# Kernel optimization log

Hardware: AMD Instinct MI355X
Metric: run time of the kernel (lower is better)

The kernel has to match this reference:

```python
import jax, jax.numpy as jnp
import numpy as np

MARGIN = 1.0
MAX_TRIALS = 50


def setup_inputs() -> dict:
    key = jax.random.key(0)
    k1, k2 = jax.random.split(key)
    B = 1048576
    scores = jax.random.normal(k1, (B,), dtype=jnp.float32)
    labels = jax.random.randint(k2, (B,), 0, 2, dtype=jnp.int64)
    return {"scores": scores, "labels": labels}


def reference(scores, labels):
    # Vectorized WARP: the sequential rejection-sampling loop draws i.i.d.
    # uniform negatives until a margin violation; equivalently we pre-draw
    # max_trials negatives per example and take the first violating one.
    B = scores.shape[0]
    lab = labels.astype(jnp.int32)
    num_pos = jnp.sum(lab == 1)
    num_neg = jnp.sum(lab == 0)

    # stable argsort puts label-0 (negative) positions first
    order = jnp.argsort(lab)

    key = jax.random.key(42)
    u = jax.random.uniform(key, (B, MAX_TRIALS), dtype=jnp.float32)
    # uniform index into the negative pool (num_neg is traced -> use floor(u*n))
    idx = jnp.minimum((u * num_neg.astype(jnp.float32)).astype(jnp.int32),
                      jnp.maximum(num_neg - 1, 0))
    neg_idx = order[idx]                       # (B, T) positions of sampled negatives
    neg_samples = scores[neg_idx]              # (B, T)

    violates = neg_samples + MARGIN > scores[:, None]   # (B, T)
    any_viol = jnp.any(violates, axis=1)
    trials = jnp.argmax(violates, axis=1)      # number of failed trials before hit
    neg_at = jnp.take_along_axis(neg_samples, trials[:, None], axis=1)[:, 0]

    # rank_est = max(1, max_trials // (trials + 1)); weight = H(rank_est)
    rank_est = jnp.maximum(1, MAX_TRIALS // (trials + 1))
    harmonics = jnp.cumsum(1.0 / jnp.arange(1, MAX_TRIALS + 1, dtype=scores.dtype))
    weight = harmonics[rank_est - 1]

    per = weight * jnp.maximum(MARGIN - (scores - neg_at), 0.0)
    per = jnp.where((lab == 1) & any_viol, per, 0.0)
    total = jnp.sum(per)

    valid = (num_pos > 0) & (num_neg > 0)
    return jnp.where(valid, total / jnp.maximum(num_pos, 1).astype(scores.dtype), 0.0)
```

## Files before the change

kernel.cpp:

```cpp
#include <hip/hip_runtime.h>
#include <stdint.h>

#define MAX_TRIALS 50
#define MARGIN 1.0f

#define SBLOCK 256
#define SEG 1024
#define MBLOCK 1024
#define MME 2
#define MCHUNK (MBLOCK * MME)

#define FLAG_AGG 1ULL
#define FLAG_INC 2ULL

__device__ __forceinline__ uint32_t rotl32(uint32_t x, uint32_t d) {
  return (x << d) | (x >> (32u - d));
}

__device__ __forceinline__ uint32_t threefry_0_42(uint32_t x0, uint32_t x1, int which) {
  const uint32_t k0 = 0u, k1 = 42u;
  const uint32_t k2 = k0 ^ k1 ^ 0x1BD11BDAu;
  const uint32_t ks[3] = {k0, k1, k2};
  const uint32_t rotA[4] = {13u, 15u, 26u, 6u};
  const uint32_t rotB[4] = {17u, 29u, 16u, 24u};
  x0 += ks[0];
  x1 += ks[1];
#pragma unroll
  for (int r = 0; r < 5; ++r) {
#pragma unroll
    for (int j = 0; j < 4; ++j) {
      uint32_t rot = (r & 1) ? rotB[j] : rotA[j];
      x0 += x1;
      x1 = rotl32(x1, rot);
      x1 ^= x0;
    }
    x0 += ks[(r + 1) % 3];
    x1 += ks[(r + 2) % 3] + (uint32_t)(r + 1);
  }
  return which ? x1 : x0;
}

__device__ __forceinline__ float sample_u(uint32_t j, uint32_t half) {
  uint32_t x0, x1;
  int which;
  if (j < half) { x0 = j; x1 = j + half; which = 0; }
  else          { x0 = j - half; x1 = j; which = 1; }
  uint32_t bits = threefry_0_42(x0, x1, which);
  return __uint_as_float((bits >> 9) | 0x3f800000u) - 1.0f;
}

__global__ void __launch_bounds__(SBLOCK) scan_scatter_kernel(
    const float* __restrict__ scores, const int* __restrict__ labels,
    unsigned long long* __restrict__ desc, int* __restrict__ counters,
    float* __restrict__ negScores, float* __restrict__ out, int B, int nseg) {
  __shared__ int s_scan[SBLOCK];
  __shared__ int s_base;
  const int t = threadIdx.x;
  const int seg = blockIdx.x;

  if (seg == 0 && t == 0) out[0] = 0.0f;

  int e0 = seg * SEG + 4 * t;
  int lab[4] = {1, 1, 1, 1};
  float sc[4] = {0.f, 0.f, 0.f, 0.f};
  if (e0 + 3 < B) {
    int4 L = *reinterpret_cast<const int4*>(labels + e0);
    float4 S = *reinterpret_cast<const float4*>(scores + e0);
    lab[0] = L.x; lab[1] = L.y; lab[2] = L.z; lab[3] = L.w;
    sc[0] = S.x; sc[1] = S.y; sc[2] = S.z; sc[3] = S.w;
  } else {
    for (int k = 0; k < 4; ++k) {
      int e = e0 + k;
      if (e < B) { lab[k] = labels[e]; sc[k] = scores[e]; }
    }
  }
  int c = (lab[0] == 0) + (lab[1] == 0) + (lab[2] == 0) + (lab[3] == 0);
  s_scan[t] = c;
  __syncthreads();
  for (int d = 1; d < SBLOCK; d <<= 1) {
    int v = (t >= d) ? s_scan[t - d] : 0;
    __syncthreads();
    s_scan[t] += v;
    __syncthreads();
  }
  const int cnt = s_scan[SBLOCK - 1];

  if (seg == 0) {
    if (t == 0) {
      atomicExch(&desc[0], (FLAG_INC << 32) | (unsigned)cnt);
      s_base = 0;
      if (nseg == 1) counters[0] = cnt;
    }
  } else {
    if (t == 0) atomicExch(&desc[seg], (FLAG_AGG << 32) | (unsigned)cnt);
    if (t < 64) {
      int running = 0;
      int w = 0;
      bool done = false;
      while (!done) {
        int idx = seg - 1 - w * 64 - t;
        unsigned flag;
        int val;
        do {
          if (idx >= 0) {
            unsigned long long v = atomicAdd(&desc[idx], 0ULL);
            flag = (unsigned)(v >> 32);
            val = (int)(unsigned)v;
          } else {
            flag = (unsigned)FLAG_INC;
            val = 0;
          }
        } while (!__all(flag == 1u || flag == 2u));
        unsigned long long incmask = __ballot(flag == 2u);
        int contrib;
        if (incmask) {
          int l = __ffsll(incmask) - 1;
          contrib = (t <= l) ? val : 0;
          done = true;
        } else {
          contrib = val;
          ++w;
        }
#pragma unroll
        for (int off = 32; off > 0; off >>= 1) contrib += __shfl_down(contrib, off, 64);
        if (t == 0) running += contrib;
      }
      if (t == 0) {
        atomicExch(&desc[seg], (FLAG_INC << 32) | (unsigned)(running + cnt));
        s_base = running;
        if (seg == nseg - 1) counters[0] = running + cnt;
      }
    }
  }
  __syncthreads();
  const int base = s_base;

  int pos = base + s_scan[t] - c;
  for (int k = 0; k < 4; ++k)
    if (lab[k] == 0) negScores[pos++] = sc[k];
}

__global__ void __launch_bounds__(MBLOCK, 8) warp_main(
    const float* __restrict__ scores, const int* __restrict__ labels,
    const float* __restrict__ negScores, const int* __restrict__ counters,
    float* __restrict__ out, int B) {
  __shared__ float H[MAX_TRIALS + 1];
  __shared__ int s_qe[MCHUNK];
  __shared__ float s_qs[MCHUNK];
  __shared__ int s_qn;
  __shared__ float s_bsum[MBLOCK / 64];

  const int tid = threadIdx.x;
  const int lane = tid & 63;
  const int wave = tid >> 6;

  if (tid == 0) {
    float a = 0.0f;
    for (int k = 1; k <= MAX_TRIALS; ++k) { a += 1.0f / (float)k; H[k] = a; }
    s_qn = 0;
  }
  __syncthreads();

  const int num_neg = counters[0];
  if (num_neg == 0) return;

  const float fneg = (float)num_neg;
  const uint32_t half = (uint32_t)(((unsigned long long)B * MAX_TRIALS) >> 1);

  float acc = 0.0f;
  int my_e[MME];
  float my_s[MME];
  int nsurv = 0;

  int e0 = blockIdx.x * MCHUNK + 2 * tid;
  int lab[2] = {1, 1};
  float sc[2] = {0.f, 0.f};
  if (e0 + 1 < B) {
    int2 L = *reinterpret_cast<const int2*>(labels + e0);
    float2 S = *reinterpret_cast<const float2*>(scores + e0);
    lab[0] = L.x; lab[1] = L.y;
    sc[0] = S.x; sc[1] = S.y;
  } else {
    for (int k = 0; k < 2; ++k) {
      int e = e0 + k;
      if (e < B) { lab[k] = labels[e]; sc[k] = scores[e]; }
    }
  }
  float n0[2], n1[2];
#pragma unroll
  for (int k = 0; k < 2; ++k) {
    if (lab[k] == 1) {
      uint32_t jb = (uint32_t)(e0 + k) * (uint32_t)MAX_TRIALS;
      float u0 = sample_u(jb, half);
      float u1 = sample_u(jb + 1u, half);
      int i0 = (int)(u0 * fneg);
      int i1 = (int)(u1 * fneg);
      if (i0 > num_neg - 1) i0 = num_neg - 1;
      if (i1 > num_neg - 1) i1 = num_neg - 1;
      n0[k] = negScores[i0];
      n1[k] = negScores[i1];
    }
  }
#pragma unroll
  for (int k = 0; k < 2; ++k) {
    if (lab[k] == 1) {
      float s = sc[k];
      if (n0[k] + MARGIN > s) {
        float h = MARGIN - (s - n0[k]);
        if (h < 0.0f) h = 0.0f;
        acc += H[50] * h;
      } else if (n1[k] + MARGIN > s) {
        float h = MARGIN - (s - n1[k]);
        if (h < 0.0f) h = 0.0f;
        acc += H[25] * h;
      } else {
        my_e[nsurv] = e0 + k;
        my_s[nsurv] = s;
        ++nsurv;
      }
    }
  }

  int qp = 0;
  if (nsurv) qp = atomicAdd(&s_qn, nsurv);
  for (int i = 0; i < nsurv; ++i) {
    s_qe[qp + i] = my_e[i];
    s_qs[qp + i] = my_s[i];
  }
  __syncthreads();

  const int qn = s_qn;
  for (int q = wave; q < qn; q += MBLOCK / 64) {
    float sq = s_qs[q];
    int eq = s_qe[q];
    int t = 2 + lane;
    bool viol = false;
    float neg = 0.0f;
    if (t < MAX_TRIALS) {
      float u = sample_u((uint32_t)eq * (uint32_t)MAX_TRIALS + (uint32_t)t, half);
      int idx = (int)(u * fneg);
      if (idx > num_neg - 1) idx = num_neg - 1;
      neg = negScores[idx];
      viol = (neg + MARGIN > sq);
    }
    unsigned long long vm = __ballot(viol);
    if (vm) {
      int f = __ffsll(vm) - 1;
      if (lane == f) {
        int trials = 2 + f;
        int rank = MAX_TRIALS / (trials + 1);
        if (rank < 1) rank = 1;
        float h = MARGIN - (sq - neg);
        if (h < 0.0f) h = 0.0f;
        acc += H[rank] * h;
      }
    }
  }

  float v = acc;
#pragma unroll
  for (int off = 32; off > 0; off >>= 1) v += __shfl_down(v, off, 64);
  if (lane == 0) s_bsum[wave] = v;
  __syncthreads();
  if (tid == 0) {
    int np = B - num_neg;
    if (np > 0) {
      float bs = 0.0f;
      for (int i = 0; i < MBLOCK / 64; ++i) bs += s_bsum[i];
      atomicAdd(out, bs * (1.0f / (float)np));
    }
  }
}

extern "C" void kernel_launch(void* const* d_in, const int* in_sizes, int n_in,
                              void* d_out, int out_size, void* d_ws, size_t ws_size,
                              hipStream_t stream) {
  const float* scores = (const float*)d_in[0];
  const int* labels = (const int*)d_in[1];
  int B = in_sizes[0];
  int nseg = (B + SEG - 1) / SEG;
  int nb2 = (B + MCHUNK - 1) / MCHUNK;

  char* ws = (char*)d_ws;
  int* counters = (int*)ws;
  unsigned long long* desc = (unsigned long long*)(ws + 64);
  float* negScores = (float*)(ws + 64 + 8 * 1024);

  scan_scatter_kernel<<<nseg, SBLOCK, 0, stream>>>(scores, labels, desc, counters,
                                                   negScores, (float*)d_out, B, nseg);
  warp_main<<<nb2, MBLOCK, 0, stream>>>(scores, labels, negScores, counters,
                                        (float*)d_out, B);
}
```

Before: 89.53 us.

## Compact positive examples during scan and spread them evenly across main-kernel blocks

After: 94.09 us. 5.1% more time.

```diff
diff --git a/kernel.cpp b/kernel.cpp
--- a/kernel.cpp
+++ b/kernel.cpp
@@ -52,7 +52,8 @@
 __global__ void __launch_bounds__(SBLOCK) scan_scatter_kernel(
     const float* __restrict__ scores, const int* __restrict__ labels,
     unsigned long long* __restrict__ desc, int* __restrict__ counters,
-    float* __restrict__ negScores, float* __restrict__ out, int B, int nseg) {
+    float* __restrict__ negScores, int* __restrict__ posE,
+    float* __restrict__ posS, float* __restrict__ out, int B, int nseg) {
   __shared__ int s_scan[SBLOCK];
   __shared__ int s_base;
   const int t = threadIdx.x;
@@ -135,13 +136,24 @@
   __syncthreads();
   const int base = s_base;
 
-  int pos = base + s_scan[t] - c;
-  for (int k = 0; k < 4; ++k)
-    if (lab[k] == 0) negScores[pos++] = sc[k];
+  int negRank = base + s_scan[t] - c;
+  for (int k = 0; k < 4; ++k) {
+    int e = e0 + k;
+    if (e < B) {
+      if (lab[k] == 0) {
+        negScores[negRank] = sc[k];
+        ++negRank;
+      } else {
+        int pi = e - negRank;
+        posE[pi] = e;
+        posS[pi] = sc[k];
+      }
+    }
+  }
 }
 
 __global__ void __launch_bounds__(MBLOCK, 8) warp_main(
-    const float* __restrict__ scores, const int* __restrict__ labels,
+    const int* __restrict__ posE, const float* __restrict__ posS,
     const float* __restrict__ negScores, const int* __restrict__ counters,
     float* __restrict__ out, int B) {
   __shared__ float H[MAX_TRIALS + 1];
@@ -163,48 +175,57 @@
 
   const int num_neg = counters[0];
   if (num_neg == 0) return;
+  const int np = B - num_neg;
+  if (np <= 0) return;
 
   const float fneg = (float)num_neg;
   const uint32_t half = (uint32_t)(((unsigned long long)B * MAX_TRIALS) >> 1);
+
+  const int nb = (int)gridDim.x;
+  int chunk = (((np + nb - 1) / nb) + 1) & ~1;
+  const int p0 = blockIdx.x * chunk;
+  const int p1 = min(p0 + chunk, np);
 
   float acc = 0.0f;
   int my_e[MME];
   float my_s[MME];
   int nsurv = 0;
 
-  int e0 = blockIdx.x * MCHUNK + 2 * tid;
-  int lab[2] = {1, 1};
-  float sc[2] = {0.f, 0.f};
-  if (e0 + 1 < B) {
-    int2 L = *reinterpret_cast<const int2*>(labels + e0);
-    float2 S = *reinterpret_cast<const float2*>(scores + e0);
-    lab[0] = L.x; lab[1] = L.y;
-    sc[0] = S.x; sc[1] = S.y;
+  const int i0 = p0 + 2 * tid;
+  int pe[2];
+  float ps[2];
+  bool val[2] = {false, false};
+  if (i0 + 1 < p1) {
+    int2 E = *reinterpret_cast<const int2*>(posE + i0);
+    float2 S = *reinterpret_cast<const float2*>(posS + i0);
+    pe[0] = E.x; pe[1] = E.y;
+    ps[0] = S.x; ps[1] = S.y;
+    val[0] = val[1] = true;
   } else {
     for (int k = 0; k < 2; ++k) {
-      int e = e0 + k;
-      if (e < B) { lab[k] = labels[e]; sc[k] = scores[e]; }
-    }
-  }
+      if (i0 + k < p1) { pe[k] = posE[i0 + k]; ps[k] = posS[i0 + k]; val[k] = true; }
+    }
+  }
+
   float n0[2], n1[2];
 #pragma unroll
   for (int k = 0; k < 2; ++k) {
-    if (lab[k] == 1) {
-      uint32_t jb = (uint32_t)(e0 + k) * (uint32_t)MAX_TRIALS;
+    if (val[k]) {
+      uint32_t jb = (uint32_t)pe[k] * (uint32_t)MAX_TRIALS;
       float u0 = sample_u(jb, half);
       float u1 = sample_u(jb + 1u, half);
-      int i0 = (int)(u0 * fneg);
-      int i1 = (int)(u1 * fneg);
-      if (i0 > num_neg - 1) i0 = num_neg - 1;
-      if (i1 > num_neg - 1) i1 = num_neg - 1;
-      n0[k] = negScores[i0];
-      n1[k] = negScores[i1];
+      int g0 = (int)(u0 * fneg);
+      int g1 = (int)(u1 * fneg);
+      if (g0 > num_neg - 1) g0 = num_neg - 1;
+      if (g1 > num_neg - 1) g1 = num_neg - 1;
+      n0[k] = negScores[g0];
+      n1[k] = negScores[g1];
     }
   }
 #pragma unroll
   for (int k = 0; k < 2; ++k) {
-    if (lab[k] == 1) {
-      float s = sc[k];
+    if (val[k]) {
+      float s = ps[k];
       if (n0[k] + MARGIN > s) {
         float h = MARGIN - (s - n0[k]);
         if (h < 0.0f) h = 0.0f;
@@ -214,7 +235,7 @@
         if (h < 0.0f) h = 0.0f;
         acc += H[25] * h;
       } else {
-        my_e[nsurv] = e0 + k;
+        my_e[nsurv] = pe[k];
         my_s[nsurv] = s;
         ++nsurv;
       }
@@ -263,12 +284,9 @@
   if (lane == 0) s_bsum[wave] = v;
   __syncthreads();
   if (tid == 0) {
-    int np = B - num_neg;
-    if (np > 0) {
-      float bs = 0.0f;
-      for (int i = 0; i < MBLOCK / 64; ++i) bs += s_bsum[i];
-      atomicAdd(out, bs * (1.0f / (float)np));
-    }
+    float bs = 0.0f;
+    for (int i = 0; i < MBLOCK / 64; ++i) bs += s_bsum[i];
+    atomicAdd(out, bs * (1.0f / (float)np));
   }
 }
 
@@ -284,10 +302,14 @@
   char* ws = (char*)d_ws;
   int* counters = (int*)ws;
   unsigned long long* desc = (unsigned long long*)(ws + 64);
-  float* negScores = (float*)(ws + 64 + 8 * 1024);
+  char* p = ws + 64 + 8192;
+  int* posE = (int*)p;
+  float* posS = (float*)(p + (size_t)B * 4);
+  float* negScores = (float*)(p + (size_t)B * 8);
 
   scan_scatter_kernel<<<nseg, SBLOCK, 0, stream>>>(scores, labels, desc, counters,
-                                                   negScores, (float*)d_out, B, nseg);
-  warp_main<<<nb2, MBLOCK, 0, stream>>>(scores, labels, negScores, counters,
+                                                   negScores, posE, posS,
+                                                   (float*)d_out, B, nseg);
+  warp_main<<<nb2, MBLOCK, 0, stream>>>(posE, posS, negScores, counters,
                                         (float*)d_out, B);
 }
```
